# Performance work log

Hardware: AMD Instinct MI355X
Metric: run time of the kernel (lower is better)

The kernel has to match this reference:

```python
import jax, jax.numpy as jnp
import numpy as np

B, S, H = 4, 512, 256

def setup_inputs() -> dict:
    key = jax.random.key(0)
    k1, k2, k3, k4 = jax.random.split(key, 4)
    scale = 1.0 / np.sqrt(H)
    return {
        "h": jax.random.normal(k1, (B, S, H), dtype=jnp.float32),
        "W_t": jax.random.normal(k2, (H, H), dtype=jnp.float32) * scale,
        "W_t_prime": jax.random.normal(k3, (H, H), dtype=jnp.float32) * scale,
        "b_h": jnp.zeros((H,), dtype=jnp.float32),
        "W_a": jax.random.normal(k4, (H,), dtype=jnp.float32) * scale,
        "b_a": jnp.zeros((), dtype=jnp.float32),
    }

def reference(h, W_t, W_t_prime, b_h, W_a, b_a):
    # Project once per timestep, then broadcast-add over the (t, t') pair grid.
    ht = jnp.einsum("bsh,hk->bsk", h, W_t)          # W_t applied to h^t
    htp = jnp.einsum("bsh,hk->bsk", h, W_t_prime)   # W_{t'} applied to h^{t'}
    # transformed: (B, S_t, S_t', H)
    transformed = ht[:, :, None, :] + htp[:, None, :, :] + b_h
    tanh_out = jnp.tanh(transformed)
    scores = jnp.einsum("bsth,h->bst", tanh_out, W_a) + b_a  # (B, S, S)
    scores = jax.nn.sigmoid(scores)
    attention_weights = jax.nn.softmax(scores, axis=2)
    output = jnp.einsum("bst,bth->bsh", attention_weights, h)
    return output, attention_weights
```

## Files before the change

kernel.cpp:

```cpp
#include <hip/hip_runtime.h>

#define Bn 4
#define Sn 512
#define Hn 256

#define CC   2.8853900817779268f
#define L2E  1.4426950408889634f

typedef __attribute__((ext_vector_type(4))) float f32x4;
typedef __attribute__((ext_vector_type(8))) short short8;

__device__ __forceinline__ unsigned short bf16rn(float f) {
    unsigned int u = __float_as_uint(f);
    u += 0x7fffu + ((u >> 16) & 1u);
    return (unsigned short)(u >> 16);
}
__device__ __forceinline__ float bf16tof(unsigned short b) {
    return __uint_as_float(((unsigned int)b) << 16);
}

__global__ __launch_bounds__(512, 4) void gemm_kernel(
    const float* __restrict__ h,  const float* __restrict__ Wt,
    const float* __restrict__ Wp, const float* __restrict__ Wa,
    const float* __restrict__ ba, const float* __restrict__ bh,
    float* __restrict__ Egt, float* __restrict__ Egp4,
    float* __restrict__ wa2, float* __restrict__ cst)
{
    __shared__ char lds[60944];
    unsigned short* A1 = (unsigned short*)lds;
    unsigned short* A2 = (unsigned short*)(lds + 8704);
    unsigned short* B1 = (unsigned short*)(lds + 17408);
    unsigned short* B2 = (unsigned short*)(lds + 34816);
    float* tile = (float*)(lds + 52224);
    float* red4 = (float*)(lds + 60928);

    const int tid = threadIdx.x;
    const int mb  = blockIdx.x >> 3;
    const int nb  = blockIdx.x & 7;
    const int m0  = mb * 32;
    const bool isT = (nb < 4);
    const int n0  = (isT ? nb : nb - 4) * 64;
    const float* __restrict__ W = isT ? Wt : Wp;

    if (blockIdx.x == 0) {
        if (tid < 256) {
            float wv = Wa[tid];
#pragma unroll
            for (int off = 32; off >= 1; off >>= 1) wv += __shfl_xor(wv, off, 64);
            if ((tid & 63) == 0) red4[tid >> 6] = wv;
        }
        __syncthreads();
        if (tid < 256) wa2[tid] = -2.0f * Wa[tid];
        if (tid == 0)
            cst[0] = -L2E * ((red4[0] + red4[1] + red4[2] + red4[3]) + ba[0]);
    }

    const int w    = tid >> 6;
    const int w2   = w & 3;
    const int mh   = w >> 2;
    const int lane = tid & 63;
    const int quad = lane >> 4;
    const int l15  = lane & 15;

    f32x4 acc = (f32x4){0.f, 0.f, 0.f, 0.f};

    for (int kh2 = 0; kh2 < 2; kh2++) {
        const int K0 = kh2 << 7;
        __syncthreads();

        {
            const int row = tid >> 4;
            const int seg = (tid & 15) * 8;
            const float* __restrict__ src = h + (m0 + row) * Hn + K0 + seg;
            unsigned int* d1 = (unsigned int*)A1 + row * 68 + (seg >> 1);
            unsigned int* d2 = (unsigned int*)A2 + row * 68 + (seg >> 1);
#pragma unroll
            for (int i = 0; i < 2; i++) {
                const float4 v = ((const float4*)src)[i];
                const float f[4] = {v.x, v.y, v.z, v.w};
                unsigned short b1[4], b2[4];
#pragma unroll
                for (int j = 0; j < 4; j++) {
                    b1[j] = bf16rn(f[j]);
                    b2[j] = bf16rn(f[j] - bf16tof(b1[j]));
                }
                d1[2 * i]     = (unsigned)b1[0] | ((unsigned)b1[1] << 16);
                d1[2 * i + 1] = (unsigned)b1[2] | ((unsigned)b1[3] << 16);
                d2[2 * i]     = (unsigned)b2[0] | ((unsigned)b2[1] << 16);
                d2[2 * i + 1] = (unsigned)b2[2] | ((unsigned)b2[3] << 16);
            }
        }

        for (int kt = 0; kt < 4; kt++) {
            const int koff = K0 + kt * 32;
            if (kt) __syncthreads();
            {
                const int kr = tid >> 4;
                const int nq = tid & 15;
                *(float4*)&tile[kr * 68 + nq * 4] =
                    *(const float4*)&W[(koff + kr) * Hn + n0 + nq * 4];
            }
            __syncthreads();
            {
                const int n  = tid >> 3;
                const int p0 = (tid & 7) * 2;
                const float f0 = tile[(2 * p0    ) * 68 + n];
                const float f1 = tile[(2 * p0 + 1) * 68 + n];
                const float f2 = tile[(2 * p0 + 2) * 68 + n];
                const float f3 = tile[(2 * p0 + 3) * 68 + n];
                const unsigned short a0 = bf16rn(f0), a1 = bf16rn(f1);
                const unsigned short a2 = bf16rn(f2), a3 = bf16rn(f3);
                const unsigned short c0 = bf16rn(f0 - bf16tof(a0));
                const unsigned short c1 = bf16rn(f1 - bf16tof(a1));
                const unsigned short c2 = bf16rn(f2 - bf16tof(a2));
                const unsigned short c3 = bf16rn(f3 - bf16tof(a3));
                unsigned int* o1 = (unsigned int*)B1 + n * 68 + kt * 16 + p0;
                unsigned int* o2 = (unsigned int*)B2 + n * 68 + kt * 16 + p0;
                o1[0] = (unsigned)a0 | ((unsigned)a1 << 16);
                o1[1] = (unsigned)a2 | ((unsigned)a3 << 16);
                o2[0] = (unsigned)c0 | ((unsigned)c1 << 16);
                o2[1] = (unsigned)c2 | ((unsigned)c3 << 16);
            }
        }
        __syncthreads();

#pragma unroll
        for (int ks = 0; ks < 128; ks += 32) {
            const int bof = (w2 * 16 + l15) * 136 + ks + quad * 8;
            const short8 b1 = *(const short8*)(B1 + bof);
            const short8 b2 = *(const short8*)(B2 + bof);
            const int aof = (mh * 16 + l15) * 136 + ks + quad * 8;
            const short8 a1 = *(const short8*)(A1 + aof);
            const short8 a2 = *(const short8*)(A2 + aof);
            acc = __builtin_amdgcn_mfma_f32_16x16x32_bf16(a1, b1, acc, 0, 0, 0);
            acc = __builtin_amdgcn_mfma_f32_16x16x32_bf16(a1, b2, acc, 0, 0, 0);
            acc = __builtin_amdgcn_mfma_f32_16x16x32_bf16(a2, b1, acc, 0, 0, 0);
        }
    }

    float* ct = tile;
#pragma unroll
    for (int r = 0; r < 4; r++)
        ct[(mh * 16 + quad * 4 + r) * 68 + w2 * 16 + l15] = acc[r];
    __syncthreads();

    const int b  = m0 >> 9;
    const int s0 = m0 & 511;
    if (isT) {
        const int n0g = nb * 64;
        const int mr = tid >> 4, nq = tid & 15;
        const float4 c  = *(const float4*)&ct[mr * 68 + nq * 4];
        const float4 bv = *(const float4*)&bh[n0g + nq * 4];
        float4 o;
        o.x = __builtin_amdgcn_exp2f((c.x + bv.x) * CC);
        o.y = __builtin_amdgcn_exp2f((c.y + bv.y) * CC);
        o.z = __builtin_amdgcn_exp2f((c.z + bv.z) * CC);
        o.w = __builtin_amdgcn_exp2f((c.w + bv.w) * CC);
        *(float4*)&Egt[(m0 + mr) * Hn + n0g + nq * 4] = o;
    } else {
        const int kq0 = (nb - 4) * 16;
        const int mr = tid & 31, nq = tid >> 5;
        const float4 c = *(const float4*)&ct[mr * 68 + nq * 4];
        float4 o;
        o.x = __builtin_amdgcn_exp2f(c.x * CC);
        o.y = __builtin_amdgcn_exp2f(c.y * CC);
        o.z = __builtin_amdgcn_exp2f(c.z * CC);
        o.w = __builtin_amdgcn_exp2f(c.w * CC);
        *(float4*)&Egp4[b * 131072 + (kq0 + nq) * 2048 + (s0 + mr) * 4] = o;
    }
}

__global__ __launch_bounds__(1024) void attn_kernel(
    const float* __restrict__ hsrc, const float* __restrict__ Egt,
    const float* __restrict__ Egp4, const float* __restrict__ wa2,
    const float* __restrict__ cst,
    float* __restrict__ out, float* __restrict__ out_attn)
{
    __shared__ char smem[40960];
    float*  attn_l = (float*)smem;
    float*  accl   = (float*)(smem + 8192);
    float*  red    = (float*)(smem + 16384);
    float4* part   = (float4*)(smem + 8192);

    const int tid = threadIdx.x;
    const int tp  = tid & 511;
    const int kh  = tid >> 9;
    const int b   = blockIdx.x & 3;
    const int t0  = (blockIdx.x >> 2) << 2;

    const int kbu = __builtin_amdgcn_readfirstlane(kh << 5);

    const float* __restrict__ egt = Egt + (b * Sn + t0) * Hn;
    const float4* __restrict__ ep = (const float4*)(Egp4 + b * (Hn * Sn));

    float acc[4] = {0.f, 0.f, 0.f, 0.f};

    float4 w4c  = *(const float4*)&wa2[kbu * 4];
    float4 eg0c = *(const float4*)&egt[0 * Hn + kbu * 4];
    float4 eg1c = *(const float4*)&egt[1 * Hn + kbu * 4];
    float4 eg2c = *(const float4*)&egt[2 * Hn + kbu * 4];
    float4 eg3c = *(const float4*)&egt[3 * Hn + kbu * 4];

#pragma unroll 2
    for (int kk = 0; kk < 32; kk++) {
        const int k4n = kbu + ((kk + 1) & 31);
        const float4 w4n  = *(const float4*)&wa2[k4n * 4];
        const float4 eg0n = *(const float4*)&egt[0 * Hn + k4n * 4];
        const float4 eg1n = *(const float4*)&egt[1 * Hn + k4n * 4];
        const float4 eg2n = *(const float4*)&egt[2 * Hn + k4n * 4];
        const float4 eg3n = *(const float4*)&egt[3 * Hn + k4n * 4];

        const float4 cur = ep[(kbu + kk) * Sn + tp];

        const float4 egs[4] = {eg0c, eg1c, eg2c, eg3c};
#pragma unroll
        for (int r = 0; r < 4; r++) {
            const float4 eg = egs[r];
            const float d1 = fmaf(cur.x, eg.x, 1.0f);
            const float d2 = fmaf(cur.y, eg.y, 1.0f);
            const float d3 = fmaf(cur.z, eg.z, 1.0f);
            const float d4 = fmaf(cur.w, eg.w, 1.0f);
            const float p12 = d1 * d2, p34 = d3 * d4;
            const float n12 = fmaf(w4c.x, d2, w4c.y * d1);
            const float n34 = fmaf(w4c.z, d4, w4c.w * d3);
            const float num = fmaf(n12, p34, n34 * p12);
            acc[r] = fmaf(num, __builtin_amdgcn_rcpf(p12 * p34), acc[r]);
        }

        w4c = w4n; eg0c = eg0n; eg1c = eg1n; eg2c = eg2n; eg3c = eg3n;
    }

    if (kh == 1) {
        accl[0 * 512 + tp] = acc[0];
        accl[1 * 512 + tp] = acc[1];
    } else {
        accl[2 * 512 + tp] = acc[2];
        accl[3 * 512 + tp] = acc[3];
    }
    __syncthreads();

    float ex[2];
    const float k0 = cst[0];
    const int  r0 = kh << 1;
    {
#pragma unroll
        for (int i = 0; i < 2; i++) {
            const int r = r0 + i;
            const float a   = acc[r] + accl[r * 512 + tp];
            const float e1  = __builtin_amdgcn_exp2f(fmaf(-L2E, a, k0));
            const float sig = __builtin_amdgcn_rcpf(1.0f + e1);
            ex[i] = __builtin_amdgcn_exp2f(L2E * sig);
        }
        const int lane = tid & 63, widl = (tid >> 6) & 7;
#pragma unroll
        for (int i = 0; i < 2; i++) {
            float v = ex[i];
#pragma unroll
            for (int off = 32; off >= 1; off >>= 1) v += __shfl_xor(v, off, 64);
            if (lane == 0) red[(r0 + i) * 8 + widl] = v;
        }
    }
    __syncthreads();

    {
#pragma unroll
        for (int i = 0; i < 2; i++) {
            const int r = r0 + i;
            float tot = 0.f;
#pragma unroll
            for (int j = 0; j < 8; j++) tot += red[r * 8 + j];
            const float a = ex[i] * __builtin_amdgcn_rcpf(tot);
            attn_l[r * Sn + tp] = a;
            out_attn[(b * Sn + t0 + r) * Sn + tp] = a;
        }
    }
    __syncthreads();

    const int c4 = tid & 63;
    const int q  = tid >> 6;

    const float* __restrict__ hb = hsrc + (b * Sn + q * 32) * Hn + c4 * 4;

    float4 a4[4];
#pragma unroll
    for (int r = 0; r < 4; r++) a4[r] = (float4){0.f, 0.f, 0.f, 0.f};

#pragma unroll 2
    for (int j4 = 0; j4 < 8; j4++) {
        float4 wv[4];
#pragma unroll
        for (int r = 0; r < 4; r++)
            wv[r] = *(const float4*)&attn_l[r * Sn + q * 32 + j4 * 4];
#pragma unroll
        for (int i = 0; i < 4; i++) {
            const float4 hv = *(const float4*)&hb[(j4 * 4 + i) * Hn];
#pragma unroll
            for (int r = 0; r < 4; r++) {
                const float wr = ((const float*)&wv[r])[i];
                a4[r].x = fmaf(wr, hv.x, a4[r].x);
                a4[r].y = fmaf(wr, hv.y, a4[r].y);
                a4[r].z = fmaf(wr, hv.z, a4[r].z);
                a4[r].w = fmaf(wr, hv.w, a4[r].w);
            }
        }
    }
    __syncthreads();

    if (q < 8) {
#pragma unroll
        for (int r = 0; r < 4; r++) part[(q * 4 + r) * 64 + c4] = a4[r];
    }
    __syncthreads();
    if (q >= 8) {
#pragma unroll
        for (int r = 0; r < 4; r++) {
            float4 p = part[((q - 8) * 4 + r) * 64 + c4];
            p.x += a4[r].x; p.y += a4[r].y; p.z += a4[r].z; p.w += a4[r].w;
            part[((q - 8) * 4 + r) * 64 + c4] = p;
        }
    }
    __syncthreads();

    {
        const int col = tid & 255;
        const int r   = tid >> 8;
        const float* pf = (const float*)part;
        float s = 0.f;
#pragma unroll
        for (int qq = 0; qq < 8; qq++)
            s += pf[((qq * 4 + r) * 64 + (col >> 2)) * 4 + (col & 3)];
        out[(b * Sn + t0 + r) * Hn + col] = s;
    }
}

extern "C" void kernel_launch(void* const* d_in, const int* in_sizes, int n_in,
                              void* d_out, int out_size, void* d_ws, size_t ws_size,
                              hipStream_t stream) {
    const float* h   = (const float*)d_in[0];
    const float* Wt  = (const float*)d_in[1];
    const float* Wtp = (const float*)d_in[2];
    const float* bh  = (const float*)d_in[3];
    const float* Wa  = (const float*)d_in[4];
    const float* ba  = (const float*)d_in[5];

    float* out      = (float*)d_out;
    float* out_attn = out + Bn * Sn * Hn;

    float* ws   = (float*)d_ws;
    float* Egt  = ws;
    float* Egp4 = ws + 524288;
    float* wa2  = ws + 1048576;
    float* cst  = ws + 1048832;

    gemm_kernel<<<dim3(512), dim3(512), 0, stream>>>(
        h, Wt, Wtp, Wa, ba, bh, Egt, Egp4, wa2, cst);
    attn_kernel<<<dim3(Bn * (Sn / 4)), dim3(1024), 0, stream>>>(
        h, Egt, Egp4, wa2, cst, out, out_attn);
}
```

Before: 112.4 us.

## Shrink attention blocks to two rows and 512 threads without K-split

The attention kernel now handles two query rows per block with 512 threads and launches twice as many blocks. Each thread covers the full hidden dimension, so the split-K LDS exchange and one barrier go away, and the two-stage partial-sum merge in the output product is simplified. The trade-off is that each Egp4 load is reused across two rows instead of four, which roughly doubles global/L2 traffic on that tensor. Each thread also runs a longer serial loop, in exchange for higher occupancy.

```diff
diff --git a/kernel.cpp b/kernel.cpp
--- a/kernel.cpp
+++ b/kernel.cpp
@@ -170,51 +170,41 @@
     }
 }
 
-__global__ __launch_bounds__(1024) void attn_kernel(
+__global__ __launch_bounds__(512, 8) void attn_kernel(
     const float* __restrict__ hsrc, const float* __restrict__ Egt,
     const float* __restrict__ Egp4, const float* __restrict__ wa2,
     const float* __restrict__ cst,
     float* __restrict__ out, float* __restrict__ out_attn)
 {
-    __shared__ char smem[40960];
-    float*  attn_l = (float*)smem;
-    float*  accl   = (float*)(smem + 8192);
-    float*  red    = (float*)(smem + 16384);
-    float4* part   = (float4*)(smem + 8192);
+    __shared__ float  attn_l[2 * 512];
+    __shared__ float  red[16];
+    __shared__ float4 part[8 * 2 * 64];
 
     const int tid = threadIdx.x;
-    const int tp  = tid & 511;
-    const int kh  = tid >> 9;
     const int b   = blockIdx.x & 3;
-    const int t0  = (blockIdx.x >> 2) << 2;
-
-    const int kbu = __builtin_amdgcn_readfirstlane(kh << 5);
+    const int t0  = (blockIdx.x >> 2) << 1;
 
     const float* __restrict__ egt = Egt + (b * Sn + t0) * Hn;
     const float4* __restrict__ ep = (const float4*)(Egp4 + b * (Hn * Sn));
 
-    float acc[4] = {0.f, 0.f, 0.f, 0.f};
-
-    float4 w4c  = *(const float4*)&wa2[kbu * 4];
-    float4 eg0c = *(const float4*)&egt[0 * Hn + kbu * 4];
-    float4 eg1c = *(const float4*)&egt[1 * Hn + kbu * 4];
-    float4 eg2c = *(const float4*)&egt[2 * Hn + kbu * 4];
-    float4 eg3c = *(const float4*)&egt[3 * Hn + kbu * 4];
+    float acc[2] = {0.f, 0.f};
+
+    float4 w4c  = *(const float4*)&wa2[0];
+    float4 eg0c = *(const float4*)&egt[0 * Hn];
+    float4 eg1c = *(const float4*)&egt[1 * Hn];
 
 #pragma unroll 2
-    for (int kk = 0; kk < 32; kk++) {
-        const int k4n = kbu + ((kk + 1) & 31);
+    for (int kk = 0; kk < 64; kk++) {
+        const int k4n = (kk + 1) & 63;
         const float4 w4n  = *(const float4*)&wa2[k4n * 4];
         const float4 eg0n = *(const float4*)&egt[0 * Hn + k4n * 4];
         const float4 eg1n = *(const float4*)&egt[1 * Hn + k4n * 4];
-        const float4 eg2n = *(const float4*)&egt[2 * Hn + k4n * 4];
-        const float4 eg3n = *(const float4*)&egt[3 * Hn + k4n * 4];
-
-        const float4 cur = ep[(kbu + kk) * Sn + tp];
-
-        const float4 egs[4] = {eg0c, eg1c, eg2c, eg3c};
-#pragma unroll
-        for (int r = 0; r < 4; r++) {
+
+        const float4 cur = ep[kk * Sn + tid];
+
+        const float4 egs[2] = {eg0c, eg1c};
+#pragma unroll
+        for (int r = 0; r < 2; r++) {
             const float4 eg = egs[r];
             const float d1 = fmaf(cur.x, eg.x, 1.0f);
             const float d2 = fmaf(cur.y, eg.y, 1.0f);
@@ -227,75 +217,59 @@
             acc[r] = fmaf(num, __builtin_amdgcn_rcpf(p12 * p34), acc[r]);
         }
 
-        w4c = w4n; eg0c = eg0n; eg1c = eg1n; eg2c = eg2n; eg3c = eg3n;
-    }
-
-    if (kh == 1) {
-        accl[0 * 512 + tp] = acc[0];
-        accl[1 * 512 + tp] = acc[1];
-    } else {
-        accl[2 * 512 + tp] = acc[2];
-        accl[3 * 512 + tp] = acc[3];
-    }
-    __syncthreads();
+        w4c = w4n; eg0c = eg0n; eg1c = eg1n;
+    }
 
     float ex[2];
     const float k0 = cst[0];
-    const int  r0 = kh << 1;
-    {
-#pragma unroll
-        for (int i = 0; i < 2; i++) {
-            const int r = r0 + i;
-            const float a   = acc[r] + accl[r * 512 + tp];
-            const float e1  = __builtin_amdgcn_exp2f(fmaf(-L2E, a, k0));
-            const float sig = __builtin_amdgcn_rcpf(1.0f + e1);
-            ex[i] = __builtin_amdgcn_exp2f(L2E * sig);
-        }
-        const int lane = tid & 63, widl = (tid >> 6) & 7;
-#pragma unroll
-        for (int i = 0; i < 2; i++) {
-            float v = ex[i];
-#pragma unroll
-            for (int off = 32; off >= 1; off >>= 1) v += __shfl_xor(v, off, 64);
-            if (lane == 0) red[(r0 + i) * 8 + widl] = v;
-        }
+#pragma unroll
+    for (int i = 0; i < 2; i++) {
+        const float a   = acc[i];
+        const float e1  = __builtin_amdgcn_exp2f(fmaf(-L2E, a, k0));
+        const float sig = __builtin_amdgcn_rcpf(1.0f + e1);
+        ex[i] = __builtin_amdgcn_exp2f(L2E * sig);
+    }
+    const int lane = tid & 63, wid = tid >> 6;
+#pragma unroll
+    for (int i = 0; i < 2; i++) {
+        float v = ex[i];
+#pragma unroll
+        for (int off = 32; off >= 1; off >>= 1) v += __shfl_xor(v, off, 64);
+        if (lane == 0) red[i * 8 + wid] = v;
     }
     __syncthreads();
 
-    {
-#pragma unroll
-        for (int i = 0; i < 2; i++) {
-            const int r = r0 + i;
-            float tot = 0.f;
-#pragma unroll
-            for (int j = 0; j < 8; j++) tot += red[r * 8 + j];
-            const float a = ex[i] * __builtin_amdgcn_rcpf(tot);
-            attn_l[r * Sn + tp] = a;
-            out_attn[(b * Sn + t0 + r) * Sn + tp] = a;
-        }
+#pragma unroll
+    for (int i = 0; i < 2; i++) {
+        float tot = 0.f;
+#pragma unroll
+        for (int j = 0; j < 8; j++) tot += red[i * 8 + j];
+        const float a = ex[i] * __builtin_amdgcn_rcpf(tot);
+        attn_l[i * 512 + tid] = a;
+        out_attn[(b * Sn + t0 + i) * Sn + tid] = a;
     }
     __syncthreads();
 
     const int c4 = tid & 63;
     const int q  = tid >> 6;
 
-    const float* __restrict__ hb = hsrc + (b * Sn + q * 32) * Hn + c4 * 4;
-
-    float4 a4[4];
-#pragma unroll
-    for (int r = 0; r < 4; r++) a4[r] = (float4){0.f, 0.f, 0.f, 0.f};
+    const float* __restrict__ hb = hsrc + (b * Sn + q * 64) * Hn + c4 * 4;
+
+    float4 a4[2];
+#pragma unroll
+    for (int r = 0; r < 2; r++) a4[r] = (float4){0.f, 0.f, 0.f, 0.f};
 
 #pragma unroll 2
-    for (int j4 = 0; j4 < 8; j4++) {
-        float4 wv[4];
-#pragma unroll
-        for (int r = 0; r < 4; r++)
-            wv[r] = *(const float4*)&attn_l[r * Sn + q * 32 + j4 * 4];
+    for (int j4 = 0; j4 < 16; j4++) {
+        float4 wv[2];
+#pragma unroll
+        for (int r = 0; r < 2; r++)
+            wv[r] = *(const float4*)&attn_l[r * 512 + q * 64 + j4 * 4];
 #pragma unroll
         for (int i = 0; i < 4; i++) {
             const float4 hv = *(const float4*)&hb[(j4 * 4 + i) * Hn];
 #pragma unroll
-            for (int r = 0; r < 4; r++) {
+            for (int r = 0; r < 2; r++) {
                 const float wr = ((const float*)&wv[r])[i];
                 a4[r].x = fmaf(wr, hv.x, a4[r].x);
                 a4[r].y = fmaf(wr, hv.y, a4[r].y);
@@ -304,21 +278,9 @@
             }
         }
     }
-    __syncthreads();
-
-    if (q < 8) {
-#pragma unroll
-        for (int r = 0; r < 4; r++) part[(q * 4 + r) * 64 + c4] = a4[r];
-    }
-    __syncthreads();
-    if (q >= 8) {
-#pragma unroll
-        for (int r = 0; r < 4; r++) {
-            float4 p = part[((q - 8) * 4 + r) * 64 + c4];
-            p.x += a4[r].x; p.y += a4[r].y; p.z += a4[r].z; p.w += a4[r].w;
-            part[((q - 8) * 4 + r) * 64 + c4] = p;
-        }
-    }
+
+#pragma unroll
+    for (int r = 0; r < 2; r++) part[(q * 2 + r) * 64 + c4] = a4[r];
     __syncthreads();
 
     {
@@ -328,7 +290,7 @@
         float s = 0.f;
 #pragma unroll
         for (int qq = 0; qq < 8; qq++)
-            s += pf[((qq * 4 + r) * 64 + (col >> 2)) * 4 + (col & 3)];
+            s += pf[((qq * 2 + r) * 64 + (col >> 2)) * 4 + (col & 3)];
         out[(b * Sn + t0 + r) * Hn + col] = s;
     }
 }
@@ -354,6 +316,6 @@
 
     gemm_kernel<<<dim3(512), dim3(512), 0, stream>>>(
         h, Wt, Wtp, Wa, ba, bh, Egt, Egp4, wa2, cst);
-    attn_kernel<<<dim3(Bn * (Sn / 4)), dim3(1024), 0, stream>>>(
+    attn_kernel<<<dim3(Bn * (Sn / 2)), dim3(512), 0, stream>>>(
         h, Egt, Egp4, wa2, cst, out, out_attn);
 }
```

Result: slower. 122.1 us (+8.6%).
